# Kernel optimization log

Hardware: AMD Instinct MI355X
Metric: run time of the kernel (lower is better)

Reference implementation:

```python
import jax, jax.numpy as jnp
import numpy as np

N_GRAPHS = 2000
NODES_PER_GRAPH = 50
EDGES_PER_GRAPH = 800  # avg degree 16
N_NODES = N_GRAPHS * NODES_PER_GRAPH          # 100_000
N_EDGES = N_GRAPHS * EDGES_PER_GRAPH          # 1_600_000
F_IN, F_H, F_PRED = 64, 128, 512
N_STEPS = 3


def _glorot(key, shape):
    fan_in, fan_out = shape[0], shape[1]
    scale = jnp.sqrt(2.0 / (fan_in + fan_out)).astype(jnp.float32)
    return jax.random.normal(key, shape, dtype=jnp.float32) * scale


def setup_inputs() -> dict:
    key = jax.random.key(0)
    ks = jax.random.split(key, 12)
    node_features = jax.random.normal(ks[0], (N_NODES, F_IN), dtype=jnp.float32)
    edge_features = jax.random.normal(ks[1], (N_EDGES, 4), dtype=jnp.float32)  # unused by model
    # edges stay within their own graph: local ids in [0, NODES_PER_GRAPH) + graph offset
    offs = (jnp.arange(N_GRAPHS, dtype=jnp.int32) * NODES_PER_GRAPH)[:, None]  # [G,1]
    src = (jax.random.randint(ks[2], (N_GRAPHS, EDGES_PER_GRAPH), 0, NODES_PER_GRAPH, dtype=jnp.int32) + offs).reshape(-1)
    dst = (jax.random.randint(ks[3], (N_GRAPHS, EDGES_PER_GRAPH), 0, NODES_PER_GRAPH, dtype=jnp.int32) + offs).reshape(-1)
    pair_indices = jnp.stack([src, dst], axis=0)  # [2, E]
    num_nodes = jnp.full((N_GRAPHS,), NODES_PER_GRAPH, dtype=jnp.int32)
    num_edges = jnp.full((N_GRAPHS,), EDGES_PER_GRAPH, dtype=jnp.int32)
    # GCN weights: [F_IN->F_H, F_H->F_H, F_H->F_H]
    W0 = _glorot(ks[4], (F_IN, F_H)); b0 = jnp.zeros((F_H,), jnp.float32)
    W1 = _glorot(ks[5], (F_H, F_H)); b1 = jnp.zeros((F_H,), jnp.float32)
    W2 = _glorot(ks[6], (F_H, F_H)); b2 = jnp.zeros((F_H,), jnp.float32)
    Wp1 = _glorot(ks[7], (F_H, F_PRED)); bp1 = jnp.zeros((F_PRED,), jnp.float32)
    Wp2 = _glorot(ks[8], (F_PRED, 1)); bp2 = jnp.zeros((1,), jnp.float32)
    return dict(node_features=node_features, edge_features=edge_features,
                pair_indices=pair_indices, num_nodes=num_nodes, num_edges=num_edges,
                W0=W0, b0=b0, W1=W1, b1=b1, W2=W2, b2=b2,
                Wp1=Wp1, bp1=bp1, Wp2=Wp2, bp2=bp2)


def reference(node_features, edge_features, pair_indices, num_nodes, num_edges,
              W0, b0, W1, b1, W2, b2, Wp1, bp1, Wp2, bp2):
    N = node_features.shape[0]
    G = num_nodes.shape[0]
    src, dst = pair_indices[0], pair_indices[1]
    ones_e = jnp.ones(src.shape[0], dtype=jnp.float32)
    # DGL GraphConv norm='both': D_out^{-1/2} on source side, D_in^{-1/2} on dest side, degrees clamped >= 1
    deg_out = jax.ops.segment_sum(ones_e, src, num_segments=N)
    deg_in = jax.ops.segment_sum(ones_e, dst, num_segments=N)
    norm_out = jnp.clip(deg_out, 1.0) ** -0.5  # [N]
    norm_in = jnp.clip(deg_in, 1.0) ** -0.5    # [N]

    def gcn_conv(feat, W, b):
        h = (feat * norm_out[:, None]) @ W                       # [N, F_out] (W applied pre-aggregation)
        agg = jax.ops.segment_sum(h[src], dst, num_segments=N)   # neighbor sum
        return jax.nn.relu(agg * norm_in[:, None] + b)

    x = gcn_conv(node_features, W0, b0)
    x = gcn_conv(x, W1, b1)
    x = gcn_conv(x, W2, b2)  # [N, F_H]

    # AvgPooling: per-graph mean over nodes
    graph_ids = jnp.repeat(jnp.arange(G, dtype=jnp.int32), num_nodes, total_repeat_length=N)
    sums = jax.ops.segment_sum(x, graph_ids, num_segments=G)       # [G, F_H]
    means = sums / num_nodes.astype(x.dtype)[:, None]

    h = jax.nn.relu(means @ Wp1 + bp1)   # Dense(512, relu)
    out = h @ Wp2 + bp2                  # Dense(1, linear) -> [G, 1]
    return out
```

## Files before the change

### kernel.cpp

```cpp
#include <hip/hip_runtime.h>

#define NG   2000
#define NPG  50
#define EPG  800
#define F0   64
#define FH   128
#define FP   512

typedef __attribute__((ext_vector_type(8))) short  short8;
typedef __attribute__((ext_vector_type(8))) __bf16 bf16x8;
typedef __attribute__((ext_vector_type(4))) float  f32x4;
typedef unsigned short u16;
typedef unsigned int   u32;

__device__ inline u16 bf16_rne(float x) {
    u32 u = __builtin_bit_cast(u32, x);
    u += 0x7fffu + ((u >> 16) & 1u);
    return (u16)(u >> 16);
}
__device__ inline float bf16f(u16 h) {
    u32 u = ((u32)h) << 16;
    return __builtin_bit_cast(float, u);
}
__device__ inline f32x4 mfma16(short8 a, short8 b, f32x4 c) {
    return __builtin_amdgcn_mfma_f32_16x16x32_bf16(
        __builtin_bit_cast(bf16x8, a), __builtin_bit_cast(bf16x8, b), c, 0, 0, 0);
}

__device__ inline int xb_idx(int row, int col)  { return row * 128 + (col  ^ ((row  & 7) << 3)); }
__device__ inline int tb_idx(int feat, int node){ return feat * 64 + (node ^ ((feat & 7) << 3)); }
__device__ inline int ah_idx(int d, int s)      { return d * 64 + (s ^ ((d & 7) << 2)); }

__global__ __launch_bounds__(256) void pack_w(
    const float* __restrict__ W0, const float* __restrict__ W1,
    const float* __restrict__ W2, u16* __restrict__ WpH, u16* __restrict__ WpL)
{
    int t = blockIdx.x * 256 + threadIdx.x;
    if (t >= 80 * 64) return;
    int fid = t >> 6, lane = t & 63;
    const float* W; int nsub, kstep;
    if (fid < 16)      { W = W0; int r = fid;      nsub = r >> 1; kstep = r & 1; }
    else if (fid < 48) { W = W1; int r = fid - 16; nsub = r >> 2; kstep = r & 3; }
    else               { W = W2; int r = fid - 48; nsub = r >> 2; kstep = r & 3; }
    int n  = nsub * 16 + (lane & 15);
    int kb = kstep * 32 + (lane >> 4) * 8;
    size_t off = (size_t)fid * 512 + (size_t)lane * 8;
#pragma unroll
    for (int i = 0; i < 8; ++i) {
        float v = W[(size_t)(kb + i) * FH + n];
        u16 h = bf16_rne(v);
        WpH[off + i] = h;
        WpL[off + i] = bf16_rne(v - bf16f(h));
    }
}

template<int KST>
__device__ void mfma1_fn(const u16* __restrict__ WpH, const u16* __restrict__ WpL,
                         int fid0, const u16* XbH, const u16* XbL,
                         u16* TbH, u16* TbL, int lane, int mstrip, int nhalf)
{
    const int l15 = lane & 15, lk = lane >> 4;
    const int arow = mstrip * 16 + l15;
    short8 ah[KST], al[KST];
#pragma unroll
    for (int ks = 0; ks < KST; ++ks) {
        int c0 = ks * 32 + lk * 8;
        ah[ks] = *(const short8*)&XbH[xb_idx(arow, c0)];
        al[ks] = *(const short8*)&XbL[xb_idx(arow, c0)];
    }
#pragma unroll
    for (int ns = 0; ns < 4; ++ns) {
        int nsg = nhalf * 4 + ns;
        f32x4 acc = {0.f, 0.f, 0.f, 0.f};
#pragma unroll
        for (int ks = 0; ks < KST; ++ks) {
            size_t off = ((size_t)(fid0 + nsg * KST + ks)) * 512 + (size_t)lane * 8;
            short8 bh = *(const short8*)(WpH + off);
            short8 bl = *(const short8*)(WpL + off);
            acc = mfma16(ah[ks], bh, acc);
            acc = mfma16(ah[ks], bl, acc);
            acc = mfma16(al[ks], bh, acc);
        }
        int feat = nsg * 16 + l15;
        int nb   = mstrip * 16 + lk * 4;
#pragma unroll
        for (int rp = 0; rp < 2; ++rp) {
            float v0 = acc[rp * 2], v1 = acc[rp * 2 + 1];
            u16 h0 = bf16_rne(v0), h1 = bf16_rne(v1);
            u16 q0 = bf16_rne(v0 - bf16f(h0)), q1 = bf16_rne(v1 - bf16f(h1));
            int idx = tb_idx(feat, nb + rp * 2);
            *(u32*)&TbH[idx] = (u32)h0 | ((u32)h1 << 16);
            *(u32*)&TbL[idx] = (u32)q0 | ((u32)q1 << 16);
        }
    }
}

template<bool LAST>
__device__ void mfma2_fn(const float* __restrict__ bias, const u32* __restrict__ Apk,
                         const u16* TbH, const u16* TbL,
                         u16* XbH, u16* XbL, float* pool,
                         int lane, int mstrip, int nhalf)
{
    const int l15 = lane & 15, lk = lane >> 4;
    const int arow = mstrip * 16 + l15;
    const bool valid = (arow < NPG);
    const int rr = valid ? arow : 0;
    short8 ah[2], al[2];
#pragma unroll
    for (int ks = 0; ks < 2; ++ks) {
        int s0 = ks * 32 + lk * 8;
        uint4 qa = *(const uint4*)&Apk[ah_idx(rr, s0)];
        uint4 qb = *(const uint4*)&Apk[ah_idx(rr, s0 + 4)];
        if (!valid) { qa.x = qa.y = qa.z = qa.w = 0u; qb = qa; }
        u32 qs[8] = {qa.x, qa.y, qa.z, qa.w, qb.x, qb.y, qb.z, qb.w};
        short8 a_h, a_l;
#pragma unroll
        for (int i = 0; i < 8; ++i) {
            a_h[i] = (short)(qs[i] & 0xffffu);
            a_l[i] = (short)(qs[i] >> 16);
        }
        ah[ks] = a_h; al[ks] = a_l;
    }
#pragma unroll
    for (int ns = 0; ns < 4; ++ns) {
        int nsg  = nhalf * 4 + ns;
        int feat = nsg * 16 + l15;
        float bc = bias[feat];
        f32x4 acc = {0.f, 0.f, 0.f, 0.f};
#pragma unroll
        for (int ks = 0; ks < 2; ++ks) {
            short8 bh = *(const short8*)&TbH[tb_idx(feat, ks * 32 + lk * 8)];
            short8 bl = *(const short8*)&TbL[tb_idx(feat, ks * 32 + lk * 8)];
            acc = mfma16(ah[ks], bh, acc);
            acc = mfma16(ah[ks], bl, acc);
            acc = mfma16(al[ks], bh, acc);
        }
        int nb = mstrip * 16 + lk * 4;
        float vs = 0.f;
#pragma unroll
        for (int r = 0; r < 4; ++r) {
            int row = nb + r;
            float v = fmaxf(acc[r] + bc, 0.f);
            if (row >= NPG) v = 0.f;
            if (LAST) {
                vs += v;
            } else {
                u16 h = bf16_rne(v);
                XbH[xb_idx(row, feat)] = h;
                XbL[xb_idx(row, feat)] = bf16_rne(v - bf16f(h));
            }
        }
        if (LAST) {
            vs += __shfl_xor(vs, 16, 64);
            vs += __shfl_xor(vs, 32, 64);
            if (lane < 16) atomicAdd(&pool[nsg * 16 + lane], vs);
        }
    }
}

__global__ __launch_bounds__(512, 4) void gcn_fused(
    const float* __restrict__ nf, const int* __restrict__ pair,
    const int* __restrict__ num_nodes,
    const float* __restrict__ b0, const float* __restrict__ b1,
    const float* __restrict__ b2,
    const u16* __restrict__ WpH, const u16* __restrict__ WpL,
    float* __restrict__ means)
{
    __shared__ u16 XbH[64 * 128], XbL[64 * 128];
    __shared__ u16 TbH[128 * 64], TbL[128 * 64];
    __shared__ float Ahat[NPG * 64];
    __shared__ float pool[FH];
    __shared__ int   din[NPG], dout[NPG];
    __shared__ float nin[NPG], nout[NPG];

    const int tid  = threadIdx.x;
    const int g    = blockIdx.x;
    const int base = g * NPG, ebase = g * EPG;
    const int* srcp = pair;
    const int* dstp = pair + (size_t)NG * EPG;

    if (tid < NPG) { din[tid] = 0; dout[tid] = 0; }
    for (int i = tid; i < NPG * 64; i += 512) Ahat[i] = 0.f;
    if (tid < FH) pool[tid] = 0.f;
    for (int i = 3200 + tid; i < 4096; i += 512) {
        ((u32*)XbH)[i] = 0u; ((u32*)XbL)[i] = 0u;
    }
    __syncthreads();

    for (int e = tid; e < EPG; e += 512) {
        int s = srcp[ebase + e] - base, d = dstp[ebase + e] - base;
        atomicAdd(&dout[s], 1);
        atomicAdd(&din [d], 1);
        atomicAdd(&Ahat[ah_idx(d, s)], 1.0f);
    }
    for (int i = tid; i < NPG * 16; i += 512) {
        int n = i >> 4, c4 = (i & 15) * 4;
        float4 v = *(const float4*)(nf + (size_t)(base + n) * F0 + c4);
        u16 h0 = bf16_rne(v.x), h1 = bf16_rne(v.y), h2 = bf16_rne(v.z), h3 = bf16_rne(v.w);
        int idx = xb_idx(n, c4);
        *(u32*)&XbH[idx]     = (u32)h0 | ((u32)h1 << 16);
        *(u32*)&XbH[idx + 2] = (u32)h2 | ((u32)h3 << 16);
        u16 l0 = bf16_rne(v.x - bf16f(h0)), l1 = bf16_rne(v.y - bf16f(h1));
        u16 l2 = bf16_rne(v.z - bf16f(h2)), l3 = bf16_rne(v.w - bf16f(h3));
        *(u32*)&XbL[idx]     = (u32)l0 | ((u32)l1 << 16);
        *(u32*)&XbL[idx + 2] = (u32)l2 | ((u32)l3 << 16);
    }
    __syncthreads();

    if (tid < NPG) {
        nout[tid] = rsqrtf((float)max(dout[tid], 1));
        nin [tid] = rsqrtf((float)max(din [tid], 1));
    }
    __syncthreads();

    const int lane   = tid & 63;
    const int wv     = __builtin_amdgcn_readfirstlane(tid >> 6);
    const int mstrip = wv & 3, nhalf = wv >> 2;

    for (int i = tid; i < NPG * 64; i += 512) {
        int d = i >> 6, sp = i & 63;
        int s = sp ^ ((d & 7) << 2);
        float sc = (s < NPG) ? nin[d] * nout[s] : 0.f;
        float v = Ahat[i] * sc;
        u16 h = bf16_rne(v);
        u16 l = bf16_rne(v - bf16f(h));
        ((u32*)Ahat)[i] = (u32)h | ((u32)l << 16);
    }
    mfma1_fn<2>(WpH, WpL, 0, XbH, XbL, TbH, TbL, lane, mstrip, nhalf);
    __syncthreads();

    const u32* Apk = (const u32*)Ahat;
    mfma2_fn<false>(b0, Apk, TbH, TbL, XbH, XbL, pool, lane, mstrip, nhalf);
    __syncthreads();
    mfma1_fn<4>(WpH, WpL, 16, XbH, XbL, TbH, TbL, lane, mstrip, nhalf);
    __syncthreads();
    mfma2_fn<false>(b1, Apk, TbH, TbL, XbH, XbL, pool, lane, mstrip, nhalf);
    __syncthreads();
    mfma1_fn<4>(WpH, WpL, 48, XbH, XbL, TbH, TbL, lane, mstrip, nhalf);
    __syncthreads();
    mfma2_fn<true>(b2, Apk, TbH, TbL, XbH, XbL, pool, lane, mstrip, nhalf);
    __syncthreads();

    if (tid < FH) means[(size_t)g * FH + tid] = pool[tid] / (float)num_nodes[g];
}

__global__ __launch_bounds__(512) void mlp_head(
    const float* __restrict__ means, const float* __restrict__ Wp1,
    const float* __restrict__ bp1,   const float* __restrict__ Wp2,
    const float* __restrict__ bp2,   float* __restrict__ out)
{
    __shared__ float ms[8][FH];
    __shared__ float wred[8][8];
    const int tid = threadIdx.x;
    const int g0  = blockIdx.x * 8;

    for (int i = tid; i < 8 * FH; i += 512)
        ms[i >> 7][i & 127] = means[(size_t)g0 * FH + i];
    __syncthreads();

    const int f = tid;
    float acc[8];
    float bb = bp1[f];
#pragma unroll
    for (int gi = 0; gi < 8; ++gi) acc[gi] = bb;
    for (int k = 0; k < FH; ++k) {
        float w = Wp1[(size_t)k * FP + f];
#pragma unroll
        for (int gi = 0; gi < 8; ++gi) acc[gi] += ms[gi][k] * w;
    }
    float w2 = Wp2[f];
#pragma unroll
    for (int gi = 0; gi < 8; ++gi) {
        float v = fmaxf(acc[gi], 0.f) * w2;
#pragma unroll
        for (int o = 32; o > 0; o >>= 1) v += __shfl_down(v, o, 64);
        if ((tid & 63) == 0) wred[tid >> 6][gi] = v;
    }
    __syncthreads();
    if (tid < 8) {
        float s = 0.f;
#pragma unroll
        for (int w = 0; w < 8; ++w) s += wred[w][tid];
        out[g0 + tid] = s + bp2[0];
    }
}

extern "C" void kernel_launch(void* const* d_in, const int* in_sizes, int n_in,
                              void* d_out, int out_size, void* d_ws, size_t ws_size,
                              hipStream_t stream) {
    const float* nf   = (const float*)d_in[0];
    const int*   pair = (const int*)d_in[2];
    const int*   nn   = (const int*)d_in[3];
    const float* W0  = (const float*)d_in[5];  const float* b0  = (const float*)d_in[6];
    const float* W1  = (const float*)d_in[7];  const float* b1  = (const float*)d_in[8];
    const float* W2  = (const float*)d_in[9];  const float* b2  = (const float*)d_in[10];
    const float* Wp1 = (const float*)d_in[11]; const float* bp1 = (const float*)d_in[12];
    const float* Wp2 = (const float*)d_in[13]; const float* bp2 = (const float*)d_in[14];

    float* means = (float*)d_ws;
    u16*   WpH   = (u16*)((char*)d_ws + (1 << 20));
    u16*   WpL   = (u16*)((char*)d_ws + (1 << 20) + 80 * 1024);
    float* out   = (float*)d_out;

    hipLaunchKernelGGL(pack_w, dim3(20), dim3(256), 0, stream, W0, W1, W2, WpH, WpL);
    hipLaunchKernelGGL(gcn_fused, dim3(NG), dim3(512), 0, stream,
                       nf, pair, nn, b0, b1, b2, WpH, WpL, means);
    hipLaunchKernelGGL(mlp_head, dim3(NG / 8), dim3(512), 0, stream,
                       means, Wp1, bp1, Wp2, bp2, out);
}
```

Measured before the change: 101.5 us.

## Store raw edge counts as exact bf16 and fold degree norms into epilogues

After: 86.71 us. 1.17x faster.

```diff
diff --git a/kernel.cpp b/kernel.cpp
--- a/kernel.cpp
+++ b/kernel.cpp
@@ -22,14 +22,25 @@
     u32 u = ((u32)h) << 16;
     return __builtin_bit_cast(float, u);
 }
+__device__ inline u32 cvtpk2(float lo, float hi) {
+    u32 r;
+    asm("v_cvt_pk_bf16_f32 %0, %1, %2" : "=v"(r) : "v"(lo), "v"(hi));
+    return r;
+}
+__device__ inline void split2(float v0, float v1, u32& hp, u32& lp) {
+    hp = cvtpk2(v0, v1);
+    float h0 = __builtin_bit_cast(float, hp << 16);
+    float h1 = __builtin_bit_cast(float, hp & 0xffff0000u);
+    lp = cvtpk2(v0 - h0, v1 - h1);
+}
 __device__ inline f32x4 mfma16(short8 a, short8 b, f32x4 c) {
     return __builtin_amdgcn_mfma_f32_16x16x32_bf16(
         __builtin_bit_cast(bf16x8, a), __builtin_bit_cast(bf16x8, b), c, 0, 0, 0);
 }
 
-__device__ inline int xb_idx(int row, int col)  { return row * 128 + (col  ^ ((row  & 7) << 3)); }
+__device__ inline int xb_idx(int row, int col)  { return row * 128 + (col ^ ((row  & 7) << 3)); }
 __device__ inline int tb_idx(int feat, int node){ return feat * 64 + (node ^ ((feat & 7) << 3)); }
-__device__ inline int ah_idx(int d, int s)      { return d * 64 + (s ^ ((d & 7) << 2)); }
+__device__ inline int ab_idx(int d, int s)      { return d * 64 + (s ^ ((d  & 7) << 3)); }
 
 __global__ __launch_bounds__(256) void pack_w(
     const float* __restrict__ W0, const float* __restrict__ W1,
@@ -57,103 +68,89 @@
 template<int KST>
 __device__ void mfma1_fn(const u16* __restrict__ WpH, const u16* __restrict__ WpL,
                          int fid0, const u16* XbH, const u16* XbL,
-                         u16* TbH, u16* TbL, int lane, int mstrip, int nhalf)
+                         u16* TbH, u16* TbL, const float* nout64,
+                         int lane, int nsg)
+{
+    const int l15 = lane & 15, lk = lane >> 4;
+    const int feat = nsg * 16 + l15;
+    short8 bh[KST], bl[KST];
+#pragma unroll
+    for (int ks = 0; ks < KST; ++ks) {
+        size_t off = (size_t)(fid0 + nsg * KST + ks) * 512 + (size_t)lane * 8;
+        bh[ks] = *(const short8*)(WpH + off);
+        bl[ks] = *(const short8*)(WpL + off);
+    }
+#pragma unroll
+    for (int ms = 0; ms < 4; ++ms) {
+        const int arow = ms * 16 + l15;
+        f32x4 acc = {0.f, 0.f, 0.f, 0.f};
+#pragma unroll
+        for (int ks = 0; ks < KST; ++ks) {
+            int c0 = ks * 32 + lk * 8;
+            short8 ah = *(const short8*)&XbH[xb_idx(arow, c0)];
+            short8 al = *(const short8*)&XbL[xb_idx(arow, c0)];
+            acc = mfma16(ah, bh[ks], acc);
+            acc = mfma16(ah, bl[ks], acc);
+            acc = mfma16(al, bh[ks], acc);
+        }
+        const int nb = ms * 16 + lk * 4;
+        float4 nq = *(const float4*)&nout64[nb];
+        u32 h01, l01, h23, l23;
+        split2(acc[0] * nq.x, acc[1] * nq.y, h01, l01);
+        split2(acc[2] * nq.z, acc[3] * nq.w, h23, l23);
+        int idx = tb_idx(feat, nb);
+        *(uint2*)&TbH[idx] = make_uint2(h01, h23);
+        *(uint2*)&TbL[idx] = make_uint2(l01, l23);
+    }
+}
+
+template<bool LAST>
+__device__ void mfma2_fn(const float* __restrict__ bias, const u16* AhB,
+                         const u16* TbH, const u16* TbL,
+                         u16* XbH, u16* XbL, float* pool, const float* nin64,
+                         int lane, int mstrip, int nhalf)
 {
     const int l15 = lane & 15, lk = lane >> 4;
     const int arow = mstrip * 16 + l15;
-    short8 ah[KST], al[KST];
-#pragma unroll
-    for (int ks = 0; ks < KST; ++ks) {
-        int c0 = ks * 32 + lk * 8;
-        ah[ks] = *(const short8*)&XbH[xb_idx(arow, c0)];
-        al[ks] = *(const short8*)&XbL[xb_idx(arow, c0)];
-    }
+    short8 a0 = *(const short8*)&AhB[ab_idx(arow, lk * 8)];
+    short8 a1 = *(const short8*)&AhB[ab_idx(arow, 32 + lk * 8)];
+    const int nb = mstrip * 16 + lk * 4;
+    float4 ninq = *(const float4*)&nin64[nb];
 #pragma unroll
     for (int ns = 0; ns < 4; ++ns) {
-        int nsg = nhalf * 4 + ns;
+        const int nsg  = nhalf * 4 + ns;
+        const int feat = nsg * 16 + l15;
+        const float bc = bias[feat];
         f32x4 acc = {0.f, 0.f, 0.f, 0.f};
-#pragma unroll
-        for (int ks = 0; ks < KST; ++ks) {
-            size_t off = ((size_t)(fid0 + nsg * KST + ks)) * 512 + (size_t)lane * 8;
-            short8 bh = *(const short8*)(WpH + off);
-            short8 bl = *(const short8*)(WpL + off);
-            acc = mfma16(ah[ks], bh, acc);
-            acc = mfma16(ah[ks], bl, acc);
-            acc = mfma16(al[ks], bh, acc);
-        }
-        int feat = nsg * 16 + l15;
-        int nb   = mstrip * 16 + lk * 4;
-#pragma unroll
-        for (int rp = 0; rp < 2; ++rp) {
-            float v0 = acc[rp * 2], v1 = acc[rp * 2 + 1];
-            u16 h0 = bf16_rne(v0), h1 = bf16_rne(v1);
-            u16 q0 = bf16_rne(v0 - bf16f(h0)), q1 = bf16_rne(v1 - bf16f(h1));
-            int idx = tb_idx(feat, nb + rp * 2);
-            *(u32*)&TbH[idx] = (u32)h0 | ((u32)h1 << 16);
-            *(u32*)&TbL[idx] = (u32)q0 | ((u32)q1 << 16);
-        }
-    }
-}
-
-template<bool LAST>
-__device__ void mfma2_fn(const float* __restrict__ bias, const u32* __restrict__ Apk,
-                         const u16* TbH, const u16* TbL,
-                         u16* XbH, u16* XbL, float* pool,
-                         int lane, int mstrip, int nhalf)
-{
-    const int l15 = lane & 15, lk = lane >> 4;
-    const int arow = mstrip * 16 + l15;
-    const bool valid = (arow < NPG);
-    const int rr = valid ? arow : 0;
-    short8 ah[2], al[2];
-#pragma unroll
-    for (int ks = 0; ks < 2; ++ks) {
-        int s0 = ks * 32 + lk * 8;
-        uint4 qa = *(const uint4*)&Apk[ah_idx(rr, s0)];
-        uint4 qb = *(const uint4*)&Apk[ah_idx(rr, s0 + 4)];
-        if (!valid) { qa.x = qa.y = qa.z = qa.w = 0u; qb = qa; }
-        u32 qs[8] = {qa.x, qa.y, qa.z, qa.w, qb.x, qb.y, qb.z, qb.w};
-        short8 a_h, a_l;
-#pragma unroll
-        for (int i = 0; i < 8; ++i) {
-            a_h[i] = (short)(qs[i] & 0xffffu);
-            a_l[i] = (short)(qs[i] >> 16);
-        }
-        ah[ks] = a_h; al[ks] = a_l;
-    }
-#pragma unroll
-    for (int ns = 0; ns < 4; ++ns) {
-        int nsg  = nhalf * 4 + ns;
-        int feat = nsg * 16 + l15;
-        float bc = bias[feat];
-        f32x4 acc = {0.f, 0.f, 0.f, 0.f};
-#pragma unroll
-        for (int ks = 0; ks < 2; ++ks) {
-            short8 bh = *(const short8*)&TbH[tb_idx(feat, ks * 32 + lk * 8)];
-            short8 bl = *(const short8*)&TbL[tb_idx(feat, ks * 32 + lk * 8)];
-            acc = mfma16(ah[ks], bh, acc);
-            acc = mfma16(ah[ks], bl, acc);
-            acc = mfma16(al[ks], bh, acc);
-        }
-        int nb = mstrip * 16 + lk * 4;
-        float vs = 0.f;
-#pragma unroll
-        for (int r = 0; r < 4; ++r) {
-            int row = nb + r;
-            float v = fmaxf(acc[r] + bc, 0.f);
-            if (row >= NPG) v = 0.f;
-            if (LAST) {
-                vs += v;
-            } else {
-                u16 h = bf16_rne(v);
-                XbH[xb_idx(row, feat)] = h;
-                XbL[xb_idx(row, feat)] = bf16_rne(v - bf16f(h));
-            }
-        }
+        short8 bh0 = *(const short8*)&TbH[tb_idx(feat, lk * 8)];
+        short8 bl0 = *(const short8*)&TbL[tb_idx(feat, lk * 8)];
+        short8 bh1 = *(const short8*)&TbH[tb_idx(feat, 32 + lk * 8)];
+        short8 bl1 = *(const short8*)&TbL[tb_idx(feat, 32 + lk * 8)];
+        acc = mfma16(a0, bh0, acc);
+        acc = mfma16(a0, bl0, acc);
+        acc = mfma16(a1, bh1, acc);
+        acc = mfma16(a1, bl1, acc);
+        float v0 = (nb + 0 < NPG) ? fmaxf(fmaf(acc[0], ninq.x, bc), 0.f) : 0.f;
+        float v1 = (nb + 1 < NPG) ? fmaxf(fmaf(acc[1], ninq.y, bc), 0.f) : 0.f;
+        float v2 = (nb + 2 < NPG) ? fmaxf(fmaf(acc[2], ninq.z, bc), 0.f) : 0.f;
+        float v3 = (nb + 3 < NPG) ? fmaxf(fmaf(acc[3], ninq.w, bc), 0.f) : 0.f;
         if (LAST) {
+            float vs = v0 + v1 + v2 + v3;
             vs += __shfl_xor(vs, 16, 64);
             vs += __shfl_xor(vs, 32, 64);
             if (lane < 16) atomicAdd(&pool[nsg * 16 + lane], vs);
+        } else {
+            u32 hp01, lp01, hp23, lp23;
+            split2(v0, v1, hp01, lp01);
+            split2(v2, v3, hp23, lp23);
+            XbH[xb_idx(nb + 0, feat)] = (u16)hp01;
+            XbH[xb_idx(nb + 1, feat)] = (u16)(hp01 >> 16);
+            XbH[xb_idx(nb + 2, feat)] = (u16)hp23;
+            XbH[xb_idx(nb + 3, feat)] = (u16)(hp23 >> 16);
+            XbL[xb_idx(nb + 0, feat)] = (u16)lp01;
+            XbL[xb_idx(nb + 1, feat)] = (u16)(lp01 >> 16);
+            XbL[xb_idx(nb + 2, feat)] = (u16)lp23;
+            XbL[xb_idx(nb + 3, feat)] = (u16)(lp23 >> 16);
         }
     }
 }
@@ -168,10 +165,12 @@
 {
     __shared__ u16 XbH[64 * 128], XbL[64 * 128];
     __shared__ u16 TbH[128 * 64], TbL[128 * 64];
-    __shared__ float Ahat[NPG * 64];
+    __shared__ u16 AhB[64 * 64];
     __shared__ float pool[FH];
     __shared__ int   din[NPG], dout[NPG];
-    __shared__ float nin[NPG], nout[NPG];
+    __shared__ float nin64[64], nout64[64];
+
+    float* cnt = (float*)TbH;
 
     const int tid  = threadIdx.x;
     const int g    = blockIdx.x;
@@ -180,8 +179,8 @@
     const int* dstp = pair + (size_t)NG * EPG;
 
     if (tid < NPG) { din[tid] = 0; dout[tid] = 0; }
-    for (int i = tid; i < NPG * 64; i += 512) Ahat[i] = 0.f;
     if (tid < FH) pool[tid] = 0.f;
+    for (int i = tid; i < 4096; i += 512) cnt[i] = 0.f;
     for (int i = 3200 + tid; i < 4096; i += 512) {
         ((u32*)XbH)[i] = 0u; ((u32*)XbL)[i] = 0u;
     }
@@ -191,54 +190,43 @@
         int s = srcp[ebase + e] - base, d = dstp[ebase + e] - base;
         atomicAdd(&dout[s], 1);
         atomicAdd(&din [d], 1);
-        atomicAdd(&Ahat[ah_idx(d, s)], 1.0f);
+        atomicAdd(&cnt[ab_idx(d, s)], 1.0f);
     }
     for (int i = tid; i < NPG * 16; i += 512) {
         int n = i >> 4, c4 = (i & 15) * 4;
         float4 v = *(const float4*)(nf + (size_t)(base + n) * F0 + c4);
-        u16 h0 = bf16_rne(v.x), h1 = bf16_rne(v.y), h2 = bf16_rne(v.z), h3 = bf16_rne(v.w);
+        u32 h01, l01, h23, l23;
+        split2(v.x, v.y, h01, l01);
+        split2(v.z, v.w, h23, l23);
         int idx = xb_idx(n, c4);
-        *(u32*)&XbH[idx]     = (u32)h0 | ((u32)h1 << 16);
-        *(u32*)&XbH[idx + 2] = (u32)h2 | ((u32)h3 << 16);
-        u16 l0 = bf16_rne(v.x - bf16f(h0)), l1 = bf16_rne(v.y - bf16f(h1));
-        u16 l2 = bf16_rne(v.z - bf16f(h2)), l3 = bf16_rne(v.w - bf16f(h3));
-        *(u32*)&XbL[idx]     = (u32)l0 | ((u32)l1 << 16);
-        *(u32*)&XbL[idx + 2] = (u32)l2 | ((u32)l3 << 16);
-    }
-    __syncthreads();
-
-    if (tid < NPG) {
-        nout[tid] = rsqrtf((float)max(dout[tid], 1));
-        nin [tid] = rsqrtf((float)max(din [tid], 1));
-    }
+        *(uint2*)&XbH[idx] = make_uint2(h01, h23);
+        *(uint2*)&XbL[idx] = make_uint2(l01, l23);
+    }
+    __syncthreads();
+
+    if (tid < 64) {
+        nout64[tid] = (tid < NPG) ? rsqrtf((float)max(dout[tid], 1)) : 0.f;
+        nin64 [tid] = (tid < NPG) ? rsqrtf((float)max(din [tid], 1)) : 0.f;
+    }
+    for (int i = tid; i < 2048; i += 512)
+        ((u32*)AhB)[i] = cvtpk2(cnt[2 * i], cnt[2 * i + 1]);
     __syncthreads();
 
     const int lane   = tid & 63;
     const int wv     = __builtin_amdgcn_readfirstlane(tid >> 6);
     const int mstrip = wv & 3, nhalf = wv >> 2;
 
-    for (int i = tid; i < NPG * 64; i += 512) {
-        int d = i >> 6, sp = i & 63;
-        int s = sp ^ ((d & 7) << 2);
-        float sc = (s < NPG) ? nin[d] * nout[s] : 0.f;
-        float v = Ahat[i] * sc;
-        u16 h = bf16_rne(v);
-        u16 l = bf16_rne(v - bf16f(h));
-        ((u32*)Ahat)[i] = (u32)h | ((u32)l << 16);
-    }
-    mfma1_fn<2>(WpH, WpL, 0, XbH, XbL, TbH, TbL, lane, mstrip, nhalf);
-    __syncthreads();
-
-    const u32* Apk = (const u32*)Ahat;
-    mfma2_fn<false>(b0, Apk, TbH, TbL, XbH, XbL, pool, lane, mstrip, nhalf);
-    __syncthreads();
-    mfma1_fn<4>(WpH, WpL, 16, XbH, XbL, TbH, TbL, lane, mstrip, nhalf);
-    __syncthreads();
-    mfma2_fn<false>(b1, Apk, TbH, TbL, XbH, XbL, pool, lane, mstrip, nhalf);
-    __syncthreads();
-    mfma1_fn<4>(WpH, WpL, 48, XbH, XbL, TbH, TbL, lane, mstrip, nhalf);
-    __syncthreads();
-    mfma2_fn<true>(b2, Apk, TbH, TbL, XbH, XbL, pool, lane, mstrip, nhalf);
+    mfma1_fn<2>(WpH, WpL, 0,  XbH, XbL, TbH, TbL, nout64, lane, wv);
+    __syncthreads();
+    mfma2_fn<false>(b0, AhB, TbH, TbL, XbH, XbL, pool, nin64, lane, mstrip, nhalf);
+    __syncthreads();
+    mfma1_fn<4>(WpH, WpL, 16, XbH, XbL, TbH, TbL, nout64, lane, wv);
+    __syncthreads();
+    mfma2_fn<false>(b1, AhB, TbH, TbL, XbH, XbL, pool, nin64, lane, mstrip, nhalf);
+    __syncthreads();
+    mfma1_fn<4>(WpH, WpL, 48, XbH, XbL, TbH, TbL, nout64, lane, wv);
+    __syncthreads();
+    mfma2_fn<true>(b2, AhB, TbH, TbL, XbH, XbL, pool, nin64, lane, mstrip, nhalf);
     __syncthreads();
 
     if (tid < FH) means[(size_t)g * FH + tid] = pool[tid] / (float)num_nodes[g];
```
